# Kernel optimization log

Measured on AMD Instinct MI355X. Metric: run time of the kernel, lower is better.

The kernel has to match this reference:

```python
import jax, jax.numpy as jnp
import numpy as np
from jax import lax

SENT_LEN = 32      # fixed sentence length used to build sent_id -> max packed length
MD = 128           # max_distance


def setup_inputs() -> dict:
    key = jax.random.key(0)
    ks = jax.random.split(key, 14)
    W, H, D, HID, E, CC, K = 4096, 2048, 768, 1024, 64, 64, 3
    PAIR = 2 * D + E  # 1600
    words = jax.random.normal(ks[0], (W, D), dtype=jnp.float32)
    sent_id = (jnp.arange(W, dtype=jnp.int32) // SENT_LEN)
    heads_ids = jax.random.randint(ks[1], (H,), 0, W, dtype=jnp.int32)
    emb_table = jax.random.normal(ks[2], (MD, E), dtype=jnp.float32) * 0.02
    w1 = jax.random.normal(ks[3], (PAIR, HID), dtype=jnp.float32) * 0.02
    b1 = jnp.zeros((HID,), jnp.float32)
    w2 = jax.random.normal(ks[4], (HID, 256), dtype=jnp.float32) * 0.02
    b2 = jnp.zeros((256,), jnp.float32)
    w3 = jax.random.normal(ks[5], (256, E), dtype=jnp.float32) * 0.02
    b3 = jnp.zeros((E,), jnp.float32)
    conv1_w = jax.random.normal(ks[6], (CC, E, K), dtype=jnp.float32) * 0.05
    conv1_b = jnp.zeros((CC,), jnp.float32)
    conv2_w = jax.random.normal(ks[7], (2, CC, K), dtype=jnp.float32) * 0.05
    conv2_b = jnp.zeros((2,), jnp.float32)
    return {"sent_id": sent_id, "words": words, "heads_ids": heads_ids,
            "emb_table": emb_table, "w1": w1, "b1": b1, "w2": w2, "b2": b2,
            "w3": w3, "b3": b3, "conv1_w": conv1_w, "conv1_b": conv1_b,
            "conv2_w": conv2_w, "conv2_b": conv2_b}


def _conv1d(x, w, b):
    # x: [N, C, L], w: [O, I, K], hardcoded padding=1 like the torch module
    y = lax.conv_general_dilated(x, w, (1,), [(1, 1)],
                                 dimension_numbers=("NCH", "OIH", "NCH"))
    return y + b[None, :, None]


def reference(sent_id, words, heads_ids, emb_table, w1, b1, w2, b2, w3, b3,
              conv1_w, conv1_b, conv2_w, conv2_b):
    H = heads_ids.shape[0]
    W = words.shape[0]
    rows = jnp.arange(H)[:, None]
    # same-sentence mask [H, W] and packed slot per column
    mask_full = sent_id[heads_ids][:, None] == sent_id[None, :]
    pos = jnp.cumsum(mask_full.astype(jnp.int32), axis=1) - 1
    slot = jnp.where(mask_full, pos, SENT_LEN)          # OOB -> dropped
    # col_idx[h, p] = word index at packed slot p (sentinel W if empty)
    col_idx = jnp.full((H, SENT_LEN), W, dtype=jnp.int32)
    col_idx = col_idx.at[rows, slot].set(
        jnp.broadcast_to(jnp.arange(W, dtype=jnp.int32)[None, :], (H, W)),
        mode="drop")
    mask = col_idx < W                                   # [H, SENT_LEN]
    cols = jnp.minimum(col_idx, W - 1)
    # gather pair features: [head feats | word feats | dist emb]
    head_w = words[heads_ids]                            # [H, D]
    word_w = words[cols]                                 # [H, L, D]
    rel = heads_ids[:, None].astype(jnp.int32) - cols    # relative positions
    eid = rel + (MD - 2) // 2
    eid = jnp.where((eid < 0) | (eid > MD - 2), MD - 1, eid)
    pairs = jnp.concatenate([
        jnp.broadcast_to(head_w[:, None, :], (H, SENT_LEN, head_w.shape[-1])),
        word_w, emb_table[eid]], axis=-1)
    pairs = jnp.where(mask[..., None], pairs, 0.0)       # torch zero padding
    # FFNN (eval mode: dropout is identity)
    x = jax.nn.relu(pairs @ w1 + b1)
    x = jax.nn.relu(x @ w2 + b2)
    x = x @ w3 + b3                                       # [H, L, E]
    # conv stack over packed word axis
    y = _conv1d(x.transpose(0, 2, 1), conv1_w, conv1_b)
    y = _conv1d(y, conv2_w, conv2_b)
    res = y.transpose(0, 2, 1)                            # [H, L, 2]
    # scatter back into full score tensor
    scores = jnp.full((H, W, 2), -jnp.inf, dtype=res.dtype)
    scores = scores.at[rows, col_idx].set(res, mode="drop")
    # eval-mode validity masks
    rel_full = heads_ids[:, None].astype(jnp.int32) - jnp.arange(W, dtype=jnp.int32)[None, :]
    valid_starts = jnp.log((rel_full >= 0).astype(scores.dtype))
    valid_ends = jnp.log((rel_full <= 0).astype(scores.dtype))
    return scores + jnp.stack([valid_starts, valid_ends], axis=2)
```

## Files before the change

kernel.cpp:

```cpp
#include <hip/hip_runtime.h>
#include <cstddef>
#include <cstdint>

#define NEG_SENT (-1.0e30f)


typedef short s8v __attribute__((ext_vector_type(8)));
typedef float f32x4 __attribute__((ext_vector_type(4)));

static __device__ __forceinline__ f32x4 mfma16(s8v a, s8v b, f32x4 c) {
  return __builtin_amdgcn_mfma_f32_16x16x32_bf16(a, b, c, 0, 0, 0);
}
static __device__ __forceinline__ unsigned short f2b(float f) {
  union { float f; unsigned u; } v{f};
  unsigned r = v.u + 0x7FFF + ((v.u >> 16) & 1);
  return (unsigned short)(r >> 16);
}
static __device__ __forceinline__ float b2f(unsigned short u) {
  union { unsigned u; float f; } v{((unsigned)u) << 16};
  return v.f;
}
static __device__ __forceinline__ unsigned pk2(float a, float b) {
#if defined(__gfx950__) && __has_builtin(__builtin_amdgcn_cvt_pk_bf16_f32)
  typedef __bf16 b2t __attribute__((ext_vector_type(2)));
  b2t r = __builtin_amdgcn_cvt_pk_bf16_f32(a, b);
  return __builtin_bit_cast(unsigned, r);
#else
  return (unsigned)f2b(a) | ((unsigned)f2b(b) << 16);
#endif
}
static __device__ __forceinline__ float blo(unsigned u) {
  union { unsigned u; float f; } v{u << 16}; return v.f;
}
static __device__ __forceinline__ float bhi(unsigned u) {
  union { unsigned u; float f; } v{u & 0xffff0000u}; return v.f;
}

__global__ __launch_bounds__(256) void k_prep0(const float* __restrict__ w1,
                                               s8v* __restrict__ w1F) {
  const int tid = blockIdx.x * 256 + threadIdx.x;
  const int lane = tid & 63, ks = (tid >> 6) % 24, nt = tid / 1536;
  const int n = nt * 16 + (lane & 15);
  const int kb = ks * 32 + 8 * (lane >> 4);
  const int z = n >> 10, col = n & 1023;
  const float* src = w1 + (size_t)(z * 768 + kb) * 1024 + col;
  s8v p;
#pragma unroll
  for (int j = 0; j < 8; ++j) p[j] = (short)f2b(src[(size_t)j * 1024]);
  w1F[tid] = p;
}

__global__ __launch_bounds__(256) void k_mid(
    const float* __restrict__ words, const s8v* __restrict__ w1F,
    unsigned short* __restrict__ AWh, unsigned short* __restrict__ AWw,
    const float* __restrict__ w1, const float* __restrict__ b1,
    const float* __restrict__ emb, const float* __restrict__ w2,
    const float* __restrict__ w3, const float* __restrict__ c1w,
    s8v* __restrict__ w2F, s8v* __restrict__ w3F, s8v* __restrict__ c1F,
    unsigned short* __restrict__ embCb, const int* __restrict__ heads,
    int* __restrict__ ord) {
  const int bx = blockIdx.x, t = threadIdx.x;
  __shared__ short As[2][8][2][64][8];
  __shared__ float se[64];
  __shared__ int hist[128], base_[128];

  if (bx < 512) {
    const int lane = t & 63, w = t >> 6;
    const int mq = w & 1, nq = w >> 1;
    const int m0 = (bx >> 4) * 128;
    const int nb = bx & 15;
    const int mA = t >> 1;
    const float* Ap = words + (size_t)(m0 + mA) * 768 + (t & 1) * 32;
    const s8v* Bp = w1F + (size_t)((nb * 8 + nq * 4) * 24) * 64 + lane;

    f32x4 acc[4][4] = {};
    float4 va[8];
    s8v bc[4][2], bn[4][2];

#pragma unroll
    for (int u = 0; u < 8; ++u) va[u] = *reinterpret_cast<const float4*>(Ap + 4 * u);
#pragma unroll
    for (int i = 0; i < 4; ++i)
#pragma unroll
      for (int ks = 0; ks < 2; ++ks) bc[i][ks] = Bp[(size_t)(i * 24 + ks) * 64];
#pragma unroll
    for (int g = 0; g < 4; ++g) {
      uint4 pu;
      pu.x = pk2(va[2 * g].x, va[2 * g].y);
      pu.y = pk2(va[2 * g].z, va[2 * g].w);
      pu.z = pk2(va[2 * g + 1].x, va[2 * g + 1].y);
      pu.w = pk2(va[2 * g + 1].z, va[2 * g + 1].w);
      *reinterpret_cast<uint4*>(&As[0][mA >> 4][t & 1][(mA & 15) + 16 * g][0]) = pu;
    }
    __syncthreads();

#pragma unroll
    for (int it = 0; it < 12; ++it) {
      const int buf = it & 1;
      if (it < 11) {
#pragma unroll
        for (int u = 0; u < 8; ++u)
          va[u] = *reinterpret_cast<const float4*>(Ap + (it + 1) * 64 + 4 * u);
#pragma unroll
        for (int i = 0; i < 4; ++i)
#pragma unroll
          for (int ks = 0; ks < 2; ++ks)
            bn[i][ks] = Bp[(size_t)(i * 24 + (it + 1) * 2 + ks) * 64];
      }
#pragma unroll
      for (int ks = 0; ks < 2; ++ks) {
        s8v a[4];
#pragma unroll
        for (int i = 0; i < 4; ++i)
          a[i] = *reinterpret_cast<const s8v*>(&As[buf][mq * 4 + i][ks][lane][0]);
#pragma unroll
        for (int i = 0; i < 4; ++i)
#pragma unroll
          for (int j = 0; j < 4; ++j)
            acc[i][j] = mfma16(a[i], bc[j][ks], acc[i][j]);
      }
      if (it < 11) {
#pragma unroll
        for (int g = 0; g < 4; ++g) {
          uint4 pu;
          pu.x = pk2(va[2 * g].x, va[2 * g].y);
          pu.y = pk2(va[2 * g].z, va[2 * g].w);
          pu.z = pk2(va[2 * g + 1].x, va[2 * g + 1].y);
          pu.w = pk2(va[2 * g + 1].z, va[2 * g + 1].w);
          *reinterpret_cast<uint4*>(
              &As[buf ^ 1][mA >> 4][t & 1][(mA & 15) + 16 * g][0]) = pu;
        }
#pragma unroll
        for (int i = 0; i < 4; ++i)
#pragma unroll
          for (int ks = 0; ks < 2; ++ks) bc[i][ks] = bn[i][ks];
      }
      __syncthreads();
    }

    const int rl = (lane >> 4) * 4, cl2 = lane & 15;
#pragma unroll
    for (int i = 0; i < 4; ++i)
#pragma unroll
      for (int j = 0; j < 4; ++j) {
        const int n = nq * 64 + j * 16 + cl2;
#pragma unroll
        for (int r = 0; r < 4; ++r) {
          const int m = m0 + mq * 64 + i * 16 + rl + r;
          if (nb < 8)
            AWh[(size_t)m * 1024 + nb * 128 + n] = f2b(acc[i][j][r]);
          else
            AWw[(size_t)m * 1024 + (nb - 8) * 128 + n] = f2b(acc[i][j][r]);
        }
      }
  } else if (bx < 654) {
    const int b = bx - 512;
    if (b < 128) {
      const int tid = b * 256 + t;
      const int lane = tid & 63, ks = (tid >> 6) % 32, nt = tid / 2048;
      const int n = nt * 16 + (lane & 15);
      const int kb = ks * 32 + 8 * (lane >> 4);
      s8v p;
#pragma unroll
      for (int j = 0; j < 8; ++j) p[j] = (short)f2b(w2[(size_t)(kb + j) * 256 + n]);
      w2F[tid] = p;
    } else if (b < 136) {
      const int tid = (b - 128) * 256 + t;
      const int lane = tid & 63, ks = (tid >> 6) % 8, nt = tid / 512;
      const int n = nt * 16 + (lane & 15);
      const int kb = ks * 32 + 8 * (lane >> 4);
      s8v p;
#pragma unroll
      for (int j = 0; j < 8; ++j) p[j] = (short)f2b(w3[(size_t)(kb + j) * 64 + n]);
      w3F[tid] = p;
    } else {
      const int tid = (b - 136) * 256 + t;
      const int lane = tid & 63, ks = (tid >> 6) % 6, nt = tid / 384;
      const int o = nt * 16 + (lane & 15);
      const int kb = ks * 32 + 8 * (lane >> 4);
      s8v p;
#pragma unroll
      for (int j = 0; j < 8; ++j) {
        const int k = kb + j, tap = k >> 6, c = k & 63;
        p[j] = (short)f2b(c1w[(size_t)(o * 64 + c) * 3 + tap]);
      }
      c1F[tid] = p;
    }
  } else if (bx < 782) {
    const int e = bx - 654;
    if (t < 64) se[t] = emb[e * 64 + t];
    __syncthreads();
    float4 acc = *reinterpret_cast<const float4*>(b1 + 4 * t);
#pragma unroll 8
    for (int d = 0; d < 64; ++d) {
      const float4 wv =
          *reinterpret_cast<const float4*>(w1 + (size_t)(1536 + d) * 1024 + 4 * t);
      const float a = se[d];
      acc.x += a * wv.x; acc.y += a * wv.y; acc.z += a * wv.z; acc.w += a * wv.w;
    }
    uint2 r; r.x = pk2(acc.x, acc.y); r.y = pk2(acc.z, acc.w);
    *reinterpret_cast<uint2*>(embCb + (size_t)e * 1024 + 4 * t) = r;
  } else {
    if (t < 128) hist[t] = 0;
    __syncthreads();
    for (int h = t; h < 2048; h += 256) atomicAdd(&hist[heads[h] >> 10 << 5 >> 5 & 127], 0);
    for (int h = t; h < 2048; h += 256) atomicAdd(&hist[(heads[h] >> 5) & 127], 1);
    __syncthreads();
    if (t == 0) {
      int s = 0;
      for (int i = 0; i < 128; ++i) { base_[i] = s; s += hist[i]; }
    }
    __syncthreads();
    for (int h = t; h < 2048; h += 256) {
      const int s = (heads[h] >> 5) & 127;
      const int p = atomicAdd(&base_[s], 1);
      ord[p] = h;
    }
  }
}

__global__ __launch_bounds__(256, 4) void k_fused(
    const int* __restrict__ heads, const int* __restrict__ ord,
    const unsigned short* __restrict__ AWh, const unsigned short* __restrict__ AWw,
    const unsigned short* __restrict__ embCb, const s8v* __restrict__ w2F,
    const float* __restrict__ b2, const s8v* __restrict__ w3F,
    const float* __restrict__ b3, const s8v* __restrict__ c1F,
    const float* __restrict__ c1b, const float* __restrict__ c2w,
    const float* __restrict__ c2b, float* __restrict__ out) {
  const int t = threadIdx.x, lane = t & 63, w = t >> 6;
  const int q = lane >> 4, cl = lane & 15;
  const int hA_ = ord[blockIdx.x * 2], hB_ = ord[blockIdx.x * 2 + 1];
  const int hidA = heads[hA_], hidB = heads[hB_];
  const int sA_ = hidA >> 5, sB_ = hidB >> 5;

  __shared__ unsigned short sHead[2][1024];
  __shared__ __align__(16) char rgn[33792];
  s8v* sB1 = reinterpret_cast<s8v*>(rgn);
  s8v (*sX2f)[8][64] = reinterpret_cast<s8v(*)[8][64]>(rgn);
  s8v (*sCv)[6][64] = reinterpret_cast<s8v(*)[6][64]>(rgn);
  unsigned short* sX2u = reinterpret_cast<unsigned short*>(rgn);
  unsigned short* sY1b = reinterpret_cast<unsigned short*>(rgn + 24576);

  {
    float4 m4; m4.x = m4.y = m4.z = m4.w = NEG_SENT;
    float4* o0 = reinterpret_cast<float4*>(out + (size_t)hA_ * 8192);
    float4* o1 = reinterpret_cast<float4*>(out + (size_t)hB_ * 8192);
#pragma unroll
    for (int i = 0; i < 8; ++i) {
      const int fi = t + (i << 8);
      if ((fi >> 4) != sA_) o0[fi] = m4;
      if ((fi >> 4) != sB_) o1[fi] = m4;
    }
  }

  {
    const uint2 ha = *reinterpret_cast<const uint2*>(AWh + (size_t)hidA * 1024 + 4 * t);
    const uint2 hb = *reinterpret_cast<const uint2*>(AWh + (size_t)hidB * 1024 + 4 * t);
    *reinterpret_cast<uint2*>(&sHead[0][4 * t]) = ha;
    *reinterpret_cast<uint2*>(&sHead[1][4 * t]) = hb;
  }

  const int kpos = (t & 15) * 8;
  const int ks2 = (t & 15) >> 2, kgs = (t & 15) & 3;
  const int slot = (t >> 4) + 16 * kgs;
  int woff[4], eoff[4], hoff[4];
#pragma unroll
  for (int r = 0; r < 4; ++r) {
    const int row = (t >> 4) + 16 * r;
    const int hd = row >> 5, pos = row & 31;
    const int hid = hd ? hidB : hidA;
    const int eid = (hid & 31) - pos + 63;
    woff[r] = ((hid >> 5) * 32 + pos) * 1024 + kpos;
    eoff[r] = eid * 1024 + kpos;
    hoff[r] = hd * 1024 + kpos;
  }

  uint4 pw[4], pe[4];
#pragma unroll
  for (int r = 0; r < 4; ++r) {
    pw[r] = *reinterpret_cast<const uint4*>(AWw + woff[r]);
    pe[r] = *reinterpret_cast<const uint4*>(embCb + eoff[r]);
  }
  __syncthreads();

  f32x4 acc[4][4] = {};

#pragma unroll
  for (int r = 0; r < 4; ++r) {
    const uint4 hv = *reinterpret_cast<const uint4*>(&sHead[0][0] + hoff[r]);
    uint4 o;
    o.x = pk2(fmaxf(blo(pw[r].x) + blo(pe[r].x) + blo(hv.x), 0.f),
              fmaxf(bhi(pw[r].x) + bhi(pe[r].x) + bhi(hv.x), 0.f));
    o.y = pk2(fmaxf(blo(pw[r].y) + blo(pe[r].y) + blo(hv.y), 0.f),
              fmaxf(bhi(pw[r].y) + bhi(pe[r].y) + bhi(hv.y), 0.f));
    o.z = pk2(fmaxf(blo(pw[r].z) + blo(pe[r].z) + blo(hv.z), 0.f),
              fmaxf(bhi(pw[r].z) + bhi(pe[r].z) + bhi(hv.z), 0.f));
    o.w = pk2(fmaxf(blo(pw[r].w) + blo(pe[r].w) + blo(hv.w), 0.f),
              fmaxf(bhi(pw[r].w) + bhi(pe[r].w) + bhi(hv.w), 0.f));
    *reinterpret_cast<uint4*>(&sB1[(size_t)(((0 * 4 + r) * 4 + ks2) * 66) + slot]) = o;
  }
  __syncthreads();

#pragma unroll
  for (int jc = 0; jc < 8; ++jc) {
    const int buf = jc & 1, nbuf = buf ^ 1;
    if (jc < 7) {
      const int j1 = (jc + 1) * 128;
#pragma unroll
      for (int r = 0; r < 4; ++r) {
        pw[r] = *reinterpret_cast<const uint4*>(AWw + woff[r] + j1);
        pe[r] = *reinterpret_cast<const uint4*>(embCb + eoff[r] + j1);
      }
    }
    const int ksg0 = jc * 4;
#pragma unroll
    for (int k2 = 0; k2 < 4; ++k2) {
      s8v av[4], bv[4];
#pragma unroll
      for (int i = 0; i < 4; ++i)
        av[i] = w2F[(size_t)((w * 4 + i) * 32 + ksg0 + k2) * 64 + lane];
#pragma unroll
      for (int ntp = 0; ntp < 4; ++ntp)
        bv[ntp] = sB1[(size_t)(((buf * 4 + ntp) * 4 + k2) * 66) + lane];
#pragma unroll
      for (int i = 0; i < 4; ++i)
#pragma unroll
        for (int ntp = 0; ntp < 4; ++ntp)
          acc[i][ntp] = mfma16(av[i], bv[ntp], acc[i][ntp]);
    }
    if (jc < 7) {
#pragma unroll
      for (int r = 0; r < 4; ++r) {
        const uint4 hv =
            *reinterpret_cast<const uint4*>(&sHead[0][0] + hoff[r] + (jc + 1) * 128);
        uint4 o;
        o.x = pk2(fmaxf(blo(pw[r].x) + blo(pe[r].x) + blo(hv.x), 0.f),
                  fmaxf(bhi(pw[r].x) + bhi(pe[r].x) + bhi(hv.x), 0.f));
        o.y = pk2(fmaxf(blo(pw[r].y) + blo(pe[r].y) + blo(hv.y), 0.f),
                  fmaxf(bhi(pw[r].y) + bhi(pe[r].y) + bhi(hv.y), 0.f));
        o.z = pk2(fmaxf(blo(pw[r].z) + blo(pe[r].z) + blo(hv.z), 0.f),
                  fmaxf(bhi(pw[r].z) + bhi(pe[r].z) + bhi(hv.z), 0.f));
        o.w = pk2(fmaxf(blo(pw[r].w) + blo(pe[r].w) + blo(hv.w), 0.f),
                  fmaxf(bhi(pw[r].w) + bhi(pe[r].w) + bhi(hv.w), 0.f));
        *reinterpret_cast<uint4*>(
            &sB1[(size_t)(((nbuf * 4 + r) * 4 + ks2) * 66) + slot]) = o;
      }
    }
    __syncthreads();
  }

#pragma unroll
  for (int i = 0; i < 4; ++i) {
    const int n2b = w * 64 + i * 16 + q * 4;
    const float4 bb = *reinterpret_cast<const float4*>(b2 + n2b);
    const int ks3 = n2b >> 5, g3 = (n2b >> 3) & 3, idx0 = n2b & 7;
#pragma unroll
    for (int ntp = 0; ntp < 4; ++ntp) {
      const unsigned u0 = pk2(fmaxf(acc[i][ntp][0] + bb.x, 0.f),
                              fmaxf(acc[i][ntp][1] + bb.y, 0.f));
      const unsigned u1 = pk2(fmaxf(acc[i][ntp][2] + bb.z, 0.f),
                              fmaxf(acc[i][ntp][3] + bb.w, 0.f));
      uint2 uu; uu.x = u0; uu.y = u1;
      *reinterpret_cast<uint2*>(
          sX2u + (((size_t)ntp * 8 + ks3) * 64 + cl + 16 * g3) * 8 + idx0) = uu;
    }
  }
  __syncthreads();

  f32x4 acc3[4] = {};
#pragma unroll
  for (int ks3 = 0; ks3 < 8; ++ks3) {
    const s8v a = w3F[(size_t)(w * 8 + ks3) * 64 + lane];
#pragma unroll
    for (int ntp = 0; ntp < 4; ++ntp)
      acc3[ntp] = mfma16(a, sX2f[ntp][ks3][lane], acc3[ntp]);
  }
  __syncthreads();

  {
    const int cb = 16 * w + q * 4;
    const float4 b3v = *reinterpret_cast<const float4*>(b3 + cb);
    const int gC = (cb >> 3) & 3, idx0 = cb & 7, ksb = cb >> 5;
#pragma unroll
    for (int ntp = 0; ntp < 4; ++ntp) {
      const int pp = ntp * 16 + cl, hd = pp >> 5, pos = pp & 31;
      const unsigned u0 = pk2(acc3[ntp][0] + b3v.x, acc3[ntp][1] + b3v.y);
      const unsigned u1 = pk2(acc3[ntp][2] + b3v.z, acc3[ntp][3] + b3v.w);
      uint2 uu; uu.x = u0; uu.y = u1;
#pragma unroll
      for (int tau = 0; tau < 3; ++tau) {
        const int pt = pos + 1 - tau;
        if ((unsigned)pt < 32u) {
          const int ppt = hd * 32 + pt;
          const int ks = 2 * tau + ksb;
          *reinterpret_cast<uint2*>(
              sX2u + (((size_t)(ppt >> 4) * 6 + ks) * 64 + (ppt & 15) + 16 * gC) * 8 +
              idx0) = uu;
        }
      }
    }
    if (t < 32) {
      const int hd = t >> 4, grp = (t >> 3) & 1;
      const int ksz = (grp ? 4 : 0) + ((t >> 2) & 1), kg = t & 3;
      const int ntpz = 2 * hd + grp, lnz = (grp ? 15 : 0) + 16 * kg;
      uint4 z; z.x = z.y = z.z = z.w = 0;
      *reinterpret_cast<uint4*>(&sCv[ntpz][ksz][lnz]) = z;
    }
  }
  __syncthreads();

  f32x4 accc[4] = {};
#pragma unroll
  for (int ks = 0; ks < 6; ++ks) {
    const s8v a = c1F[(size_t)(w * 6 + ks) * 64 + lane];
#pragma unroll
    for (int ntp = 0; ntp < 4; ++ntp)
      accc[ntp] = mfma16(a, sCv[ntp][ks][lane], accc[ntp]);
  }
  {
    const int o = t >> 2, czi = t & 3;
    const int colz = (czi == 0) ? 0 : (czi == 1) ? 33 : (czi == 2) ? 34 : 67;
    sY1b[o * 68 + colz] = 0;
  }
  {
    const int ob = 16 * w + q * 4;
    const float4 cbv = *reinterpret_cast<const float4*>(c1b + ob);
#pragma unroll
    for (int ntp = 0; ntp < 4; ++ntp) {
      const int pp = ntp * 16 + cl, hd = pp >> 5, pos = pp & 31;
      const int col = hd * 34 + 1 + pos;
      sY1b[(ob + 0) * 68 + col] = f2b(accc[ntp][0] + cbv.x);
      sY1b[(ob + 1) * 68 + col] = f2b(accc[ntp][1] + cbv.y);
      sY1b[(ob + 2) * 68 + col] = f2b(accc[ntp][2] + cbv.z);
      sY1b[(ob + 3) * 68 + col] = f2b(accc[ntp][3] + cbv.w);
    }
  }
  __syncthreads();

  {
    const int kq = t & 1, c2 = (t >> 1) & 1, pp = t >> 2;
    const int hd = pp >> 5, pos = pp & 31, col = hd * 34 + 1 + pos;
    float a2 = 0.f;
    const float* wp = c2w + (size_t)(c2 * 64 + kq * 32) * 3;
    const unsigned short* yb = sY1b + (size_t)(kq * 32) * 68 + col;
#pragma unroll
    for (int o = 0; o < 32; ++o) {
      a2 += b2f(yb[o * 68 - 1]) * wp[o * 3 + 0] +
            b2f(yb[o * 68]) * wp[o * 3 + 1] +
            b2f(yb[o * 68 + 1]) * wp[o * 3 + 2];
    }
    a2 += __shfl_xor(a2, 1, 64);
    if (kq == 0) {
      const int hR_ = hd ? hB_ : hA_;
      const int hidR = hd ? hidB : hidA;
      const int sR = hidR >> 5, offR = hidR & 31;
      const int rel = offR - pos;
      const bool ok = (c2 == 0) ? (rel >= 0) : (rel <= 0);
      out[(size_t)hR_ * 8192 + (size_t)(sR * 32 + pos) * 2 + c2] =
          ok ? (a2 + c2b[c2]) : NEG_SENT;
    }
  }
}

extern "C" void kernel_launch(void* const* d_in, const int* in_sizes, int n_in,
                              void* d_out, int out_size, void* d_ws,
                              size_t ws_size, hipStream_t stream) {
  const float* words = (const float*)d_in[1];
  const int* heads = (const int*)d_in[2];
  const float* emb = (const float*)d_in[3];
  const float* w1 = (const float*)d_in[4];
  const float* b1 = (const float*)d_in[5];
  const float* w2 = (const float*)d_in[6];
  const float* b2 = (const float*)d_in[7];
  const float* w3 = (const float*)d_in[8];
  const float* b3 = (const float*)d_in[9];
  const float* c1w = (const float*)d_in[10];
  const float* c1b = (const float*)d_in[11];
  const float* c2w = (const float*)d_in[12];
  const float* c2b = (const float*)d_in[13];
  float* out = (float*)d_out;

  char* ws = (char*)d_ws;
  unsigned short* embCb = (unsigned short*)ws;      ws += 128 * 1024 * 2;
  unsigned short* AWh = (unsigned short*)ws;        ws += 4096 * 1024 * 2;
  unsigned short* AWw = (unsigned short*)ws;        ws += 4096 * 1024 * 2;
  s8v* w1F = (s8v*)ws;                              ws += 196608 * 16;
  s8v* w2F = (s8v*)ws;                              ws += 32768 * 16;
  s8v* w3F = (s8v*)ws;                              ws += 2048 * 16;
  s8v* c1F = (s8v*)ws;                              ws += 1536 * 16;
  int* ord = (int*)ws;                              ws += 2048 * 4;

  k_prep0<<<768, 256, 0, stream>>>(w1, w1F);
  k_mid<<<783, 256, 0, stream>>>(words, w1F, AWh, AWw, w1, b1, emb, w2, w3,
                                 c1w, w2F, w3F, c1F, embCb, heads, ord);
  k_fused<<<1024, 256, 0, stream>>>(heads, ord, AWh, AWw, embCb, w2F, b2, w3F,
                                    b3, c1F, c1b, c2w, c2b, out);
}
```

Measured before the change: 234.9 us.

## Restage pipeline: pre-convert words to bf16, merge AW buffers, register-fed FFN2 GEMM

Words are converted to bf16 in the prep kernel along with all the weight repacking, so the word-projection GEMM kernel only streams bf16 operands and does no conversion. The two head and word projection outputs are merged into one interleaved buffer. The fused kernel's second FFN layer now builds its B fragments in registers straight from global memory, with each wave owning a head and a half of N, instead of staging them through double-buffered shared memory with barriers. This trades extra global reads and a larger workspace for fewer syncs and fewer conversions, and it drops the occupancy hint on the fused kernel.

```diff
diff --git a/kernel.cpp b/kernel.cpp
--- a/kernel.cpp
+++ b/kernel.cpp
@@ -36,158 +36,68 @@
   union { unsigned u; float f; } v{u & 0xffff0000u}; return v.f;
 }
 
-__global__ __launch_bounds__(256) void k_prep0(const float* __restrict__ w1,
-                                               s8v* __restrict__ w1F) {
-  const int tid = blockIdx.x * 256 + threadIdx.x;
-  const int lane = tid & 63, ks = (tid >> 6) % 24, nt = tid / 1536;
-  const int n = nt * 16 + (lane & 15);
-  const int kb = ks * 32 + 8 * (lane >> 4);
-  const int z = n >> 10, col = n & 1023;
-  const float* src = w1 + (size_t)(z * 768 + kb) * 1024 + col;
-  s8v p;
-#pragma unroll
-  for (int j = 0; j < 8; ++j) p[j] = (short)f2b(src[(size_t)j * 1024]);
-  w1F[tid] = p;
-}
-
-__global__ __launch_bounds__(256) void k_mid(
-    const float* __restrict__ words, const s8v* __restrict__ w1F,
-    unsigned short* __restrict__ AWh, unsigned short* __restrict__ AWw,
-    const float* __restrict__ w1, const float* __restrict__ b1,
-    const float* __restrict__ emb, const float* __restrict__ w2,
-    const float* __restrict__ w3, const float* __restrict__ c1w,
+__global__ __launch_bounds__(256) void k_prep0(
+    const float* __restrict__ words, const float* __restrict__ w1,
+    const float* __restrict__ b1, const float* __restrict__ emb,
+    const float* __restrict__ w2, const float* __restrict__ w3,
+    const float* __restrict__ c1w, const int* __restrict__ heads,
+    unsigned short* __restrict__ wordsB, s8v* __restrict__ w1F,
     s8v* __restrict__ w2F, s8v* __restrict__ w3F, s8v* __restrict__ c1F,
-    unsigned short* __restrict__ embCb, const int* __restrict__ heads,
-    int* __restrict__ ord) {
+    unsigned short* __restrict__ embCb, int* __restrict__ ord) {
   const int bx = blockIdx.x, t = threadIdx.x;
-  __shared__ short As[2][8][2][64][8];
   __shared__ float se[64];
   __shared__ int hist[128], base_[128];
-
-  if (bx < 512) {
-    const int lane = t & 63, w = t >> 6;
-    const int mq = w & 1, nq = w >> 1;
-    const int m0 = (bx >> 4) * 128;
-    const int nb = bx & 15;
-    const int mA = t >> 1;
-    const float* Ap = words + (size_t)(m0 + mA) * 768 + (t & 1) * 32;
-    const s8v* Bp = w1F + (size_t)((nb * 8 + nq * 4) * 24) * 64 + lane;
-
-    f32x4 acc[4][4] = {};
-    float4 va[8];
-    s8v bc[4][2], bn[4][2];
-
-#pragma unroll
-    for (int u = 0; u < 8; ++u) va[u] = *reinterpret_cast<const float4*>(Ap + 4 * u);
-#pragma unroll
-    for (int i = 0; i < 4; ++i)
-#pragma unroll
-      for (int ks = 0; ks < 2; ++ks) bc[i][ks] = Bp[(size_t)(i * 24 + ks) * 64];
-#pragma unroll
-    for (int g = 0; g < 4; ++g) {
-      uint4 pu;
-      pu.x = pk2(va[2 * g].x, va[2 * g].y);
-      pu.y = pk2(va[2 * g].z, va[2 * g].w);
-      pu.z = pk2(va[2 * g + 1].x, va[2 * g + 1].y);
-      pu.w = pk2(va[2 * g + 1].z, va[2 * g + 1].w);
-      *reinterpret_cast<uint4*>(&As[0][mA >> 4][t & 1][(mA & 15) + 16 * g][0]) = pu;
-    }
-    __syncthreads();
-
-#pragma unroll
-    for (int it = 0; it < 12; ++it) {
-      const int buf = it & 1;
-      if (it < 11) {
-#pragma unroll
-        for (int u = 0; u < 8; ++u)
-          va[u] = *reinterpret_cast<const float4*>(Ap + (it + 1) * 64 + 4 * u);
-#pragma unroll
-        for (int i = 0; i < 4; ++i)
-#pragma unroll
-          for (int ks = 0; ks < 2; ++ks)
-            bn[i][ks] = Bp[(size_t)(i * 24 + (it + 1) * 2 + ks) * 64];
-      }
-#pragma unroll
-      for (int ks = 0; ks < 2; ++ks) {
-        s8v a[4];
-#pragma unroll
-        for (int i = 0; i < 4; ++i)
-          a[i] = *reinterpret_cast<const s8v*>(&As[buf][mq * 4 + i][ks][lane][0]);
-#pragma unroll
-        for (int i = 0; i < 4; ++i)
-#pragma unroll
-          for (int j = 0; j < 4; ++j)
-            acc[i][j] = mfma16(a[i], bc[j][ks], acc[i][j]);
-      }
-      if (it < 11) {
-#pragma unroll
-        for (int g = 0; g < 4; ++g) {
-          uint4 pu;
-          pu.x = pk2(va[2 * g].x, va[2 * g].y);
-          pu.y = pk2(va[2 * g].z, va[2 * g].w);
-          pu.z = pk2(va[2 * g + 1].x, va[2 * g + 1].y);
-          pu.w = pk2(va[2 * g + 1].z, va[2 * g + 1].w);
-          *reinterpret_cast<uint4*>(
-              &As[buf ^ 1][mA >> 4][t & 1][(mA & 15) + 16 * g][0]) = pu;
-        }
-#pragma unroll
-        for (int i = 0; i < 4; ++i)
-#pragma unroll
-          for (int ks = 0; ks < 2; ++ks) bc[i][ks] = bn[i][ks];
-      }
-      __syncthreads();
-    }
-
-    const int rl = (lane >> 4) * 4, cl2 = lane & 15;
-#pragma unroll
-    for (int i = 0; i < 4; ++i)
-#pragma unroll
-      for (int j = 0; j < 4; ++j) {
-        const int n = nq * 64 + j * 16 + cl2;
-#pragma unroll
-        for (int r = 0; r < 4; ++r) {
-          const int m = m0 + mq * 64 + i * 16 + rl + r;
-          if (nb < 8)
-            AWh[(size_t)m * 1024 + nb * 128 + n] = f2b(acc[i][j][r]);
-          else
-            AWw[(size_t)m * 1024 + (nb - 8) * 128 + n] = f2b(acc[i][j][r]);
-        }
-      }
-  } else if (bx < 654) {
-    const int b = bx - 512;
-    if (b < 128) {
-      const int tid = b * 256 + t;
-      const int lane = tid & 63, ks = (tid >> 6) % 32, nt = tid / 2048;
-      const int n = nt * 16 + (lane & 15);
-      const int kb = ks * 32 + 8 * (lane >> 4);
-      s8v p;
-#pragma unroll
-      for (int j = 0; j < 8; ++j) p[j] = (short)f2b(w2[(size_t)(kb + j) * 256 + n]);
-      w2F[tid] = p;
-    } else if (b < 136) {
-      const int tid = (b - 128) * 256 + t;
-      const int lane = tid & 63, ks = (tid >> 6) % 8, nt = tid / 512;
-      const int n = nt * 16 + (lane & 15);
-      const int kb = ks * 32 + 8 * (lane >> 4);
-      s8v p;
-#pragma unroll
-      for (int j = 0; j < 8; ++j) p[j] = (short)f2b(w3[(size_t)(kb + j) * 64 + n]);
-      w3F[tid] = p;
-    } else {
-      const int tid = (b - 136) * 256 + t;
-      const int lane = tid & 63, ks = (tid >> 6) % 6, nt = tid / 384;
-      const int o = nt * 16 + (lane & 15);
-      const int kb = ks * 32 + 8 * (lane >> 4);
-      s8v p;
-#pragma unroll
-      for (int j = 0; j < 8; ++j) {
-        const int k = kb + j, tap = k >> 6, c = k & 63;
-        p[j] = (short)f2b(c1w[(size_t)(o * 64 + c) * 3 + tap]);
-      }
-      c1F[tid] = p;
-    }
-  } else if (bx < 782) {
-    const int e = bx - 654;
+  if (bx < 1536) {
+    const size_t o = (size_t)(bx * 256 + t) * 8;
+    const float4 v0 = *reinterpret_cast<const float4*>(words + o);
+    const float4 v1 = *reinterpret_cast<const float4*>(words + o + 4);
+    uint4 r;
+    r.x = pk2(v0.x, v0.y); r.y = pk2(v0.z, v0.w);
+    r.z = pk2(v1.x, v1.y); r.w = pk2(v1.z, v1.w);
+    *reinterpret_cast<uint4*>(wordsB + o) = r;
+  } else if (bx < 2304) {
+    const int tid = (bx - 1536) * 256 + t;
+    const int lane = tid & 63, ks = (tid >> 6) % 24, nt = tid / 1536;
+    const int n = nt * 16 + (lane & 15);
+    const int kb = ks * 32 + 8 * (lane >> 4);
+    const int z = n >> 10, col = n & 1023;
+    const float* src = w1 + (size_t)(z * 768 + kb) * 1024 + col;
+    s8v p;
+#pragma unroll
+    for (int j = 0; j < 8; ++j) p[j] = (short)f2b(src[(size_t)j * 1024]);
+    w1F[tid] = p;
+  } else if (bx < 2432) {
+    const int tid = (bx - 2304) * 256 + t;
+    const int lane = tid & 63, ks = (tid >> 6) % 32, nt = tid / 2048;
+    const int n = nt * 16 + (lane & 15);
+    const int kb = ks * 32 + 8 * (lane >> 4);
+    s8v p;
+#pragma unroll
+    for (int j = 0; j < 8; ++j) p[j] = (short)f2b(w2[(size_t)(kb + j) * 256 + n]);
+    w2F[tid] = p;
+  } else if (bx < 2440) {
+    const int tid = (bx - 2432) * 256 + t;
+    const int lane = tid & 63, ks = (tid >> 6) % 8, nt = tid / 512;
+    const int n = nt * 16 + (lane & 15);
+    const int kb = ks * 32 + 8 * (lane >> 4);
+    s8v p;
+#pragma unroll
+    for (int j = 0; j < 8; ++j) p[j] = (short)f2b(w3[(size_t)(kb + j) * 64 + n]);
+    w3F[tid] = p;
+  } else if (bx < 2446) {
+    const int tid = (bx - 2440) * 256 + t;
+    const int lane = tid & 63, ks = (tid >> 6) % 6, nt = tid / 384;
+    const int o = nt * 16 + (lane & 15);
+    const int kb = ks * 32 + 8 * (lane >> 4);
+    s8v p;
+#pragma unroll
+    for (int j = 0; j < 8; ++j) {
+      const int k = kb + j, tap = k >> 6, c = k & 63;
+      p[j] = (short)f2b(c1w[(size_t)(o * 64 + c) * 3 + tap]);
+    }
+    c1F[tid] = p;
+  } else if (bx < 2574) {
+    const int e = bx - 2446;
     if (t < 64) se[t] = emb[e * 64 + t];
     __syncthreads();
     float4 acc = *reinterpret_cast<const float4*>(b1 + 4 * t);
@@ -203,7 +113,6 @@
   } else {
     if (t < 128) hist[t] = 0;
     __syncthreads();
-    for (int h = t; h < 2048; h += 256) atomicAdd(&hist[heads[h] >> 10 << 5 >> 5 & 127], 0);
     for (int h = t; h < 2048; h += 256) atomicAdd(&hist[(heads[h] >> 5) & 127], 1);
     __syncthreads();
     if (t == 0) {
@@ -219,9 +128,89 @@
   }
 }
 
-__global__ __launch_bounds__(256, 4) void k_fused(
+__global__ __launch_bounds__(256) void k_mid(
+    const unsigned short* __restrict__ wordsB, const s8v* __restrict__ w1F,
+    unsigned short* __restrict__ AWb) {
+  const int bx = blockIdx.x, t = threadIdx.x;
+  __shared__ short As[2][8][2][64][8];
+  const int lane = t & 63, w = t >> 6;
+  const int mq = w & 1, nq = w >> 1;
+  const int m0 = (bx >> 4) * 128;
+  const int nb = bx & 15;
+  const int mA = t >> 1;
+  const unsigned short* Ap = wordsB + (size_t)(m0 + mA) * 768 + (t & 1) * 32;
+  const s8v* Bp = w1F + (size_t)((nb * 8 + nq * 4) * 24) * 64 + lane;
+
+  f32x4 acc[4][4] = {};
+  uint4 va[4];
+  s8v bc[4][2], bn[4][2];
+
+#pragma unroll
+  for (int u = 0; u < 4; ++u) va[u] = *reinterpret_cast<const uint4*>(Ap + 8 * u);
+#pragma unroll
+  for (int i = 0; i < 4; ++i)
+#pragma unroll
+    for (int ks = 0; ks < 2; ++ks) bc[i][ks] = Bp[(size_t)(i * 24 + ks) * 64];
+#pragma unroll
+  for (int u = 0; u < 4; ++u)
+    *reinterpret_cast<uint4*>(&As[0][mA >> 4][t & 1][(mA & 15) + 16 * u][0]) = va[u];
+  __syncthreads();
+
+#pragma unroll
+  for (int it = 0; it < 12; ++it) {
+    const int buf = it & 1;
+    if (it < 11) {
+#pragma unroll
+      for (int u = 0; u < 4; ++u)
+        va[u] = *reinterpret_cast<const uint4*>(Ap + (it + 1) * 64 + 8 * u);
+#pragma unroll
+      for (int i = 0; i < 4; ++i)
+#pragma unroll
+        for (int ks = 0; ks < 2; ++ks)
+          bn[i][ks] = Bp[(size_t)(i * 24 + (it + 1) * 2 + ks) * 64];
+    }
+#pragma unroll
+    for (int ks = 0; ks < 2; ++ks) {
+      s8v a[4];
+#pragma unroll
+      for (int i = 0; i < 4; ++i)
+        a[i] = *reinterpret_cast<const s8v*>(&As[buf][mq * 4 + i][ks][lane][0]);
+#pragma unroll
+      for (int i = 0; i < 4; ++i)
+#pragma unroll
+        for (int j = 0; j < 4; ++j)
+          acc[i][j] = mfma16(a[i], bc[j][ks], acc[i][j]);
+    }
+    if (it < 11) {
+#pragma unroll
+      for (int u = 0; u < 4; ++u)
+        *reinterpret_cast<uint4*>(
+            &As[buf ^ 1][mA >> 4][t & 1][(mA & 15) + 16 * u][0]) = va[u];
+#pragma unroll
+      for (int i = 0; i < 4; ++i)
+#pragma unroll
+        for (int ks = 0; ks < 2; ++ks) bc[i][ks] = bn[i][ks];
+    }
+    __syncthreads();
+  }
+
+  const int rl = (lane >> 4) * 4, cl2 = lane & 15;
+#pragma unroll
+  for (int i = 0; i < 4; ++i)
+#pragma unroll
+    for (int j = 0; j < 4; ++j) {
+      const int n = nq * 64 + j * 16 + cl2;
+#pragma unroll
+      for (int r = 0; r < 4; ++r) {
+        const int m = m0 + mq * 64 + i * 16 + rl + r;
+        AWb[(size_t)m * 2048 + nb * 128 + n] = f2b(acc[i][j][r]);
+      }
+    }
+}
+
+__global__ __launch_bounds__(256) void k_fused(
     const int* __restrict__ heads, const int* __restrict__ ord,
-    const unsigned short* __restrict__ AWh, const unsigned short* __restrict__ AWw,
+    const unsigned short* __restrict__ AWb,
     const unsigned short* __restrict__ embCb, const s8v* __restrict__ w2F,
     const float* __restrict__ b2, const s8v* __restrict__ w3F,
     const float* __restrict__ b3, const s8v* __restrict__ c1F,
@@ -229,16 +218,15 @@
     const float* __restrict__ c2b, float* __restrict__ out) {
   const int t = threadIdx.x, lane = t & 63, w = t >> 6;
   const int q = lane >> 4, cl = lane & 15;
+  const int ph = w >> 1, nh = w & 1;
   const int hA_ = ord[blockIdx.x * 2], hB_ = ord[blockIdx.x * 2 + 1];
   const int hidA = heads[hA_], hidB = heads[hB_];
   const int sA_ = hidA >> 5, sB_ = hidB >> 5;
 
   __shared__ unsigned short sHead[2][1024];
-  __shared__ __align__(16) char rgn[33792];
-  s8v* sB1 = reinterpret_cast<s8v*>(rgn);
-  s8v (*sX2f)[8][64] = reinterpret_cast<s8v(*)[8][64]>(rgn);
-  s8v (*sCv)[6][64] = reinterpret_cast<s8v(*)[6][64]>(rgn);
+  __shared__ __align__(16) char rgn[36864];
   unsigned short* sX2u = reinterpret_cast<unsigned short*>(rgn);
+  s8v* sFr = reinterpret_cast<s8v*>(rgn);
   unsigned short* sY1b = reinterpret_cast<unsigned short*>(rgn + 24576);
 
   {
@@ -254,112 +242,78 @@
   }
 
   {
-    const uint2 ha = *reinterpret_cast<const uint2*>(AWh + (size_t)hidA * 1024 + 4 * t);
-    const uint2 hb = *reinterpret_cast<const uint2*>(AWh + (size_t)hidB * 1024 + 4 * t);
+    const uint2 ha = *reinterpret_cast<const uint2*>(AWb + (size_t)hidA * 2048 + 4 * t);
+    const uint2 hb = *reinterpret_cast<const uint2*>(AWb + (size_t)hidB * 2048 + 4 * t);
     *reinterpret_cast<uint2*>(&sHead[0][4 * t]) = ha;
     *reinterpret_cast<uint2*>(&sHead[1][4 * t]) = hb;
   }
-
-  const int kpos = (t & 15) * 8;
-  const int ks2 = (t & 15) >> 2, kgs = (t & 15) & 3;
-  const int slot = (t >> 4) + 16 * kgs;
-  int woff[4], eoff[4], hoff[4];
-#pragma unroll
-  for (int r = 0; r < 4; ++r) {
-    const int row = (t >> 4) + 16 * r;
-    const int hd = row >> 5, pos = row & 31;
-    const int hid = hd ? hidB : hidA;
-    const int eid = (hid & 31) - pos + 63;
-    woff[r] = ((hid >> 5) * 32 + pos) * 1024 + kpos;
-    eoff[r] = eid * 1024 + kpos;
-    hoff[r] = hd * 1024 + kpos;
-  }
-
-  uint4 pw[4], pe[4];
-#pragma unroll
-  for (int r = 0; r < 4; ++r) {
-    pw[r] = *reinterpret_cast<const uint4*>(AWw + woff[r]);
-    pe[r] = *reinterpret_cast<const uint4*>(embCb + eoff[r]);
-  }
-  __syncthreads();
-
-  f32x4 acc[4][4] = {};
-
-#pragma unroll
-  for (int r = 0; r < 4; ++r) {
-    const uint4 hv = *reinterpret_cast<const uint4*>(&sHead[0][0] + hoff[r]);
-    uint4 o;
-    o.x = pk2(fmaxf(blo(pw[r].x) + blo(pe[r].x) + blo(hv.x), 0.f),
-              fmaxf(bhi(pw[r].x) + bhi(pe[r].x) + bhi(hv.x), 0.f));
-    o.y = pk2(fmaxf(blo(pw[r].y) + blo(pe[r].y) + blo(hv.y), 0.f),
-              fmaxf(bhi(pw[r].y) + bhi(pe[r].y) + bhi(hv.y), 0.f));
-    o.z = pk2(fmaxf(blo(pw[r].z) + blo(pe[r].z) + blo(hv.z), 0.f),
-              fmaxf(bhi(pw[r].z) + bhi(pe[r].z) + bhi(hv.z), 0.f));
-    o.w = pk2(fmaxf(blo(pw[r].w) + blo(pe[r].w) + blo(hv.w), 0.f),
-              fmaxf(bhi(pw[r].w) + bhi(pe[r].w) + bhi(hv.w), 0.f));
-    *reinterpret_cast<uint4*>(&sB1[(size_t)(((0 * 4 + r) * 4 + ks2) * 66) + slot]) = o;
-  }
-  __syncthreads();
-
-#pragma unroll
-  for (int jc = 0; jc < 8; ++jc) {
-    const int buf = jc & 1, nbuf = buf ^ 1;
-    if (jc < 7) {
-      const int j1 = (jc + 1) * 128;
-#pragma unroll
-      for (int r = 0; r < 4; ++r) {
-        pw[r] = *reinterpret_cast<const uint4*>(AWw + woff[r] + j1);
-        pe[r] = *reinterpret_cast<const uint4*>(embCb + eoff[r] + j1);
-      }
-    }
-    const int ksg0 = jc * 4;
-#pragma unroll
-    for (int k2 = 0; k2 < 4; ++k2) {
-      s8v av[4], bv[4];
-#pragma unroll
-      for (int i = 0; i < 4; ++i)
-        av[i] = w2F[(size_t)((w * 4 + i) * 32 + ksg0 + k2) * 64 + lane];
-#pragma unroll
-      for (int ntp = 0; ntp < 4; ++ntp)
-        bv[ntp] = sB1[(size_t)(((buf * 4 + ntp) * 4 + k2) * 66) + lane];
-#pragma unroll
-      for (int i = 0; i < 4; ++i)
-#pragma unroll
-        for (int ntp = 0; ntp < 4; ++ntp)
-          acc[i][ntp] = mfma16(av[i], bv[ntp], acc[i][ntp]);
-    }
-    if (jc < 7) {
-#pragma unroll
-      for (int r = 0; r < 4; ++r) {
-        const uint4 hv =
-            *reinterpret_cast<const uint4*>(&sHead[0][0] + hoff[r] + (jc + 1) * 128);
-        uint4 o;
-        o.x = pk2(fmaxf(blo(pw[r].x) + blo(pe[r].x) + blo(hv.x), 0.f),
-                  fmaxf(bhi(pw[r].x) + bhi(pe[r].x) + bhi(hv.x), 0.f));
-        o.y = pk2(fmaxf(blo(pw[r].y) + blo(pe[r].y) + blo(hv.y), 0.f),
-                  fmaxf(bhi(pw[r].y) + bhi(pe[r].y) + bhi(hv.y), 0.f));
-        o.z = pk2(fmaxf(blo(pw[r].z) + blo(pe[r].z) + blo(hv.z), 0.f),
-                  fmaxf(bhi(pw[r].z) + bhi(pe[r].z) + bhi(hv.z), 0.f));
-        o.w = pk2(fmaxf(blo(pw[r].w) + blo(pe[r].w) + blo(hv.w), 0.f),
-                  fmaxf(bhi(pw[r].w) + bhi(pe[r].w) + bhi(hv.w), 0.f));
-        *reinterpret_cast<uint4*>(
-            &sB1[(size_t)(((nbuf * 4 + r) * 4 + ks2) * 66) + slot]) = o;
-      }
-    }
-    __syncthreads();
-  }
-
-#pragma unroll
-  for (int i = 0; i < 4; ++i) {
-    const int n2b = w * 64 + i * 16 + q * 4;
+  __syncthreads();
+
+  const int hidP = ph ? hidB : hidA;
+  const int offP = hidP & 31;
+  const unsigned short* wp0 =
+      AWb + (size_t)((hidP >> 5) * 32 + cl) * 2048 + 1024 + 8 * q;
+  const unsigned short* wp1 = wp0 + 16 * 2048;
+  const unsigned short* ep0 = embCb + (size_t)(offP - cl + 63) * 1024 + 8 * q;
+  const unsigned short* ep1 = ep0 - (size_t)16 * 1024;
+  const unsigned short* hp = &sHead[ph][8 * q];
+  const s8v* w2p = w2F + (size_t)(nh * 8) * 32 * 64 + lane;
+
+  f32x4 acc[8][2] = {};
+  uint4 cw0 = *reinterpret_cast<const uint4*>(wp0);
+  uint4 cw1 = *reinterpret_cast<const uint4*>(wp1);
+  uint4 ce0 = *reinterpret_cast<const uint4*>(ep0);
+  uint4 ce1 = *reinterpret_cast<const uint4*>(ep1);
+  uint4 chv = *reinterpret_cast<const uint4*>(hp);
+
+#pragma unroll 4
+  for (int ks = 0; ks < 32; ++ks) {
+    uint4 b0u, b1u;
+    b0u.x = pk2(fmaxf(blo(cw0.x) + blo(ce0.x) + blo(chv.x), 0.f),
+                fmaxf(bhi(cw0.x) + bhi(ce0.x) + bhi(chv.x), 0.f));
+    b0u.y = pk2(fmaxf(blo(cw0.y) + blo(ce0.y) + blo(chv.y), 0.f),
+                fmaxf(bhi(cw0.y) + bhi(ce0.y) + bhi(chv.y), 0.f));
+    b0u.z = pk2(fmaxf(blo(cw0.z) + blo(ce0.z) + blo(chv.z), 0.f),
+                fmaxf(bhi(cw0.z) + bhi(ce0.z) + bhi(chv.z), 0.f));
+    b0u.w = pk2(fmaxf(blo(cw0.w) + blo(ce0.w) + blo(chv.w), 0.f),
+                fmaxf(bhi(cw0.w) + bhi(ce0.w) + bhi(chv.w), 0.f));
+    b1u.x = pk2(fmaxf(blo(cw1.x) + blo(ce1.x) + blo(chv.x), 0.f),
+                fmaxf(bhi(cw1.x) + bhi(ce1.x) + bhi(chv.x), 0.f));
+    b1u.y = pk2(fmaxf(blo(cw1.y) + blo(ce1.y) + blo(chv.y), 0.f),
+                fmaxf(bhi(cw1.y) + bhi(ce1.y) + bhi(chv.y), 0.f));
+    b1u.z = pk2(fmaxf(blo(cw1.z) + blo(ce1.z) + blo(chv.z), 0.f),
+                fmaxf(bhi(cw1.z) + bhi(ce1.z) + bhi(chv.z), 0.f));
+    b1u.w = pk2(fmaxf(blo(cw1.w) + blo(ce1.w) + blo(chv.w), 0.f),
+                fmaxf(bhi(cw1.w) + bhi(ce1.w) + bhi(chv.w), 0.f));
+    const s8v bv0 = __builtin_bit_cast(s8v, b0u);
+    const s8v bv1 = __builtin_bit_cast(s8v, b1u);
+    if (ks < 31) {
+      cw0 = *reinterpret_cast<const uint4*>(wp0 + 32 * (ks + 1));
+      cw1 = *reinterpret_cast<const uint4*>(wp1 + 32 * (ks + 1));
+      ce0 = *reinterpret_cast<const uint4*>(ep0 + 32 * (ks + 1));
+      ce1 = *reinterpret_cast<const uint4*>(ep1 + 32 * (ks + 1));
+      chv = *reinterpret_cast<const uint4*>(hp + 32 * (ks + 1));
+    }
+#pragma unroll
+    for (int i = 0; i < 8; ++i) {
+      const s8v av = w2p[(size_t)(i * 32 + ks) * 64];
+      acc[i][0] = mfma16(av, bv0, acc[i][0]);
+      acc[i][1] = mfma16(av, bv1, acc[i][1]);
+    }
+  }
+
+#pragma unroll
+  for (int i = 0; i < 8; ++i) {
+    const int n2b = (nh * 8 + i) * 16 + q * 4;
     const float4 bb = *reinterpret_cast<const float4*>(b2 + n2b);
     const int ks3 = n2b >> 5, g3 = (n2b >> 3) & 3, idx0 = n2b & 7;
 #pragma unroll
-    for (int ntp = 0; ntp < 4; ++ntp) {
-      const unsigned u0 = pk2(fmaxf(acc[i][ntp][0] + bb.x, 0.f),
-                              fmaxf(acc[i][ntp][1] + bb.y, 0.f));
-      const unsigned u1 = pk2(fmaxf(acc[i][ntp][2] + bb.z, 0.f),
-                              fmaxf(acc[i][ntp][3] + bb.w, 0.f));
+    for (int j = 0; j < 2; ++j) {
+      const int ntp = ph * 2 + j;
+      const unsigned u0 = pk2(fmaxf(acc[i][j][0] + bb.x, 0.f),
+                              fmaxf(acc[i][j][1] + bb.y, 0.f));
+      const unsigned u1 = pk2(fmaxf(acc[i][j][2] + bb.z, 0.f),
+                              fmaxf(acc[i][j][3] + bb.w, 0.f));
       uint2 uu; uu.x = u0; uu.y = u1;
       *reinterpret_cast<uint2*>(
           sX2u + (((size_t)ntp * 8 + ks3) * 64 + cl + 16 * g3) * 8 + idx0) = uu;
@@ -373,7 +327,7 @@
     const s8v a = w3F[(size_t)(w * 8 + ks3) * 64 + lane];
 #pragma unroll
     for (int ntp = 0; ntp < 4; ++ntp)
-      acc3[ntp] = mfma16(a, sX2f[ntp][ks3][lane], acc3[ntp]);
+      acc3[ntp] = mfma16(a, sFr[(size_t)(ntp * 8 + ks3) * 64 + lane], acc3[ntp]);
   }
   __syncthreads();
 
@@ -404,7 +358,7 @@
       const int ksz = (grp ? 4 : 0) + ((t >> 2) & 1), kg = t & 3;
       const int ntpz = 2 * hd + grp, lnz = (grp ? 15 : 0) + 16 * kg;
       uint4 z; z.x = z.y = z.z = z.w = 0;
-      *reinterpret_cast<uint4*>(&sCv[ntpz][ksz][lnz]) = z;
+      *reinterpret_cast<uint4*>(&sFr[(size_t)(ntpz * 6 + ksz) * 64 + lnz]) = z;
     }
   }
   __syncthreads();
@@ -415,7 +369,7 @@
     const s8v a = c1F[(size_t)(w * 6 + ks) * 64 + lane];
 #pragma unroll
     for (int ntp = 0; ntp < 4; ++ntp)
-      accc[ntp] = mfma16(a, sCv[ntp][ks][lane], accc[ntp]);
+      accc[ntp] = mfma16(a, sFr[(size_t)(ntp * 6 + ks) * 64 + lane], accc[ntp]);
   }
   {
     const int o = t >> 2, czi = t & 3;
@@ -441,13 +395,13 @@
     const int kq = t & 1, c2 = (t >> 1) & 1, pp = t >> 2;
     const int hd = pp >> 5, pos = pp & 31, col = hd * 34 + 1 + pos;
     float a2 = 0.f;
-    const float* wp = c2w + (size_t)(c2 * 64 + kq * 32) * 3;
+    const float* wpc = c2w + (size_t)(c2 * 64 + kq * 32) * 3;
     const unsigned short* yb = sY1b + (size_t)(kq * 32) * 68 + col;
 #pragma unroll
     for (int o = 0; o < 32; ++o) {
-      a2 += b2f(yb[o * 68 - 1]) * wp[o * 3 + 0] +
-            b2f(yb[o * 68]) * wp[o * 3 + 1] +
-            b2f(yb[o * 68 + 1]) * wp[o * 3 + 2];
+      a2 += b2f(yb[o * 68 - 1]) * wpc[o * 3 + 0] +
+            b2f(yb[o * 68]) * wpc[o * 3 + 1] +
+            b2f(yb[o * 68 + 1]) * wpc[o * 3 + 2];
     }
     a2 += __shfl_xor(a2, 1, 64);
     if (kq == 0) {
@@ -482,17 +436,17 @@
 
   char* ws = (char*)d_ws;
   unsigned short* embCb = (unsigned short*)ws;      ws += 128 * 1024 * 2;
-  unsigned short* AWh = (unsigned short*)ws;        ws += 4096 * 1024 * 2;
-  unsigned short* AWw = (unsigned short*)ws;        ws += 4096 * 1024 * 2;
+  unsigned short* AWb = (unsigned short*)ws;        ws += 4096 * 2048 * 2;
+  unsigned short* wordsB = (unsigned short*)ws;     ws += 4096 * 768 * 2;
   s8v* w1F = (s8v*)ws;                              ws += 196608 * 16;
   s8v* w2F = (s8v*)ws;                              ws += 32768 * 16;
   s8v* w3F = (s8v*)ws;                              ws += 2048 * 16;
   s8v* c1F = (s8v*)ws;                              ws += 1536 * 16;
   int* ord = (int*)ws;                              ws += 2048 * 4;
 
-  k_prep0<<<768, 256, 0, stream>>>(w1, w1F);
-  k_mid<<<783, 256, 0, stream>>>(words, w1F, AWh, AWw, w1, b1, emb, w2, w3,
-                                 c1w, w2F, w3F, c1F, embCb, heads, ord);
-  k_fused<<<1024, 256, 0, stream>>>(heads, ord, AWh, AWw, embCb, w2F, b2, w3F,
-                                    b3, c1F, c1b, c2w, c2b, out);
-}
+  k_prep0<<<2575, 256, 0, stream>>>(words, w1, b1, emb, w2, w3, c1w, heads,
+                                    wordsB, w1F, w2F, w3F, c1F, embCb, ord);
+  k_mid<<<512, 256, 0, stream>>>(wordsB, w1F, AWb);
+  k_fused<<<1024, 256, 0, stream>>>(heads, ord, AWb, embCb, w2F, b2, w3F, b3,
+                                    c1F, c1b, c2w, c2b, out);
+}
```

New measurement: 248.8 us. +5.9%, slower.
